# Performance work log

Measured on AMD Instinct MI355X. Metric: run time of the kernel, lower is better.

Reference implementation:

```python
import jax, jax.numpy as jnp
import numpy as np

TOP_K = 2
TEMP = 1.0

def setup_inputs() -> dict:
    key = jax.random.key(0)
    ks = jax.random.split(key, 7)
    B, T, D, E = 2, 2048, 768, 8
    F = 4 * D
    s = 0.02
    return {
        "x": jax.random.normal(ks[0], (B, T, D), dtype=jnp.float32),
        "gate_w": jax.random.normal(ks[1], (D, E), dtype=jnp.float32) * s,
        "gate_b": jnp.zeros((E,), dtype=jnp.float32),
        "w1": jax.random.normal(ks[2], (E, D, F), dtype=jnp.float32) * s,
        "b1": jnp.zeros((E, F), dtype=jnp.float32),
        "w2": jax.random.normal(ks[3], (E, F, D), dtype=jnp.float32) * s,
        "b2": jnp.zeros((E, D), dtype=jnp.float32),
    }

def reference(x, gate_w, gate_b, w1, b1, w2, b2):
    B, T, D = x.shape
    E = gate_w.shape[1]
    x_flat = x.reshape(-1, D)                       # [N, D]
    logits = x_flat @ gate_w + gate_b              # [N, E]
    gates = jax.nn.softmax(logits / TEMP, axis=-1)
    topk_gates, topk_idx = jax.lax.top_k(gates, TOP_K)   # [N, K]
    topk_gates = topk_gates / (jnp.sum(topk_gates, axis=-1, keepdims=True) + 1e-9)
    # Dense combine weights: w[n, e] = sum_k topk_gates[n, k] * (topk_idx[n, k] == e)
    combine = jnp.sum(
        topk_gates[:, :, None] * jax.nn.one_hot(topk_idx, E, dtype=x.dtype),
        axis=1,
    )                                               # [N, E]
    out = jnp.zeros_like(x_flat)
    for e in range(E):  # fixed small expert loop (structurally distinct params)
        h = jax.nn.gelu(x_flat @ w1[e] + b1[e], approximate=False)  # [N, 4D]
        y = h @ w2[e] + b2[e]                                       # [N, D]
        out = out + combine[:, e:e + 1] * y
    return out.reshape(B, T, D)
```

## Files before the change

### kernel.cpp

```cpp
#include <hip/hip_runtime.h>
#include <hip/hip_bf16.h>


#define N_TOK 4096
#define DIM   768
#define FDIM  3072
#define NEXP  8

typedef __attribute__((ext_vector_type(8))) _Float16 f16x8;
typedef __attribute__((ext_vector_type(4))) _Float16 f16x4;
typedef __attribute__((ext_vector_type(4))) float     f32x4;

__device__ __forceinline__ float gelu_exact(float v) {
    return 0.5f * v * (1.0f + erff(v * 0.7071067811865475f));
}

__device__ __forceinline__ void gload_lds16(const _Float16* g, _Float16* l) {
    __builtin_amdgcn_global_load_lds(
        (const __attribute__((address_space(1))) void*)g,
        (__attribute__((address_space(3))) void*)l,
        16, 0, 0);
}

__global__ __launch_bounds__(256) void cast_x_kernel(const float* __restrict__ x,
                                                     _Float16* __restrict__ xh) {
    int i = blockIdx.x * 256 + threadIdx.x;
    float4 v = ((const float4*)x)[i];
    f16x4 o;
    o[0] = (_Float16)v.x; o[1] = (_Float16)v.y;
    o[2] = (_Float16)v.z; o[3] = (_Float16)v.w;
    ((f16x4*)xh)[i] = o;
}

__global__ __launch_bounds__(256) void transpose_cast_kernel(const float* __restrict__ in,
                                                             _Float16* __restrict__ out,
                                                             int R, int C) {
    const int e  = blockIdx.z;
    const size_t eoff = (size_t)e * R * C;
    const int c0 = blockIdx.x * 64;
    const int r0 = blockIdx.y * 64;
    __shared__ _Float16 tile[64][66];
    const int t = threadIdx.x;
    #pragma unroll
    for (int it = 0; it < 4; it++) {
        int lin = it * 256 + t;
        int r  = lin >> 4;
        int c4 = lin & 15;
        float4 v = *(const float4*)&in[eoff + (size_t)(r0 + r) * C + c0 + c4 * 4];
        tile[r][c4 * 4 + 0] = (_Float16)v.x;
        tile[r][c4 * 4 + 1] = (_Float16)v.y;
        tile[r][c4 * 4 + 2] = (_Float16)v.z;
        tile[r][c4 * 4 + 3] = (_Float16)v.w;
    }
    __syncthreads();
    #pragma unroll
    for (int it = 0; it < 4; it++) {
        int lin = it * 256 + t;
        int c  = lin >> 4;
        int r4 = lin & 15;
        f16x4 o;
        #pragma unroll
        for (int j = 0; j < 4; j++) o[j] = tile[r4 * 4 + j][c];
        *(f16x4*)&out[eoff + (size_t)(c0 + c) * R + r0 + r4 * 4] = o;
    }
}

__global__ __launch_bounds__(256) void gate_kernel(const float* __restrict__ x,
                                                   const float* __restrict__ gw,
                                                   const float* __restrict__ gb,
                                                   int* __restrict__ tok_list,
                                                   float* __restrict__ wt_list,
                                                   int* __restrict__ count) {
    const int gtid = blockIdx.x * 256 + threadIdx.x;
    const int n    = gtid >> 6;
    const int lane = threadIdx.x & 63;
    if (n >= N_TOK) return;
    double part[NEXP];
    #pragma unroll
    for (int e = 0; e < NEXP; e++) part[e] = 0.0;
    for (int d = lane; d < DIM; d += 64) {
        float xv = x[n * DIM + d];
        const float* g = &gw[d * NEXP];
        #pragma unroll
        for (int e = 0; e < NEXP; e++) part[e] += (double)xv * (double)g[e];
    }
    #pragma unroll
    for (int e = 0; e < NEXP; e++) {
        double v = part[e];
        #pragma unroll
        for (int off = 32; off > 0; off >>= 1) v += __shfl_xor(v, off);
        part[e] = v + (double)gb[e];
    }
    if (lane == 0) {
        double mx = part[0];
        #pragma unroll
        for (int e = 1; e < NEXP; e++) mx = fmax(mx, part[e]);
        double ex[NEXP]; double s = 0.0;
        #pragma unroll
        for (int e = 0; e < NEXP; e++) { ex[e] = exp(part[e] - mx); s += ex[e]; }
        int i0 = 0;
        #pragma unroll
        for (int e = 1; e < NEXP; e++) if (ex[e] > ex[i0]) i0 = e;
        int i1 = (i0 == 0) ? 1 : 0;
        #pragma unroll
        for (int e = 0; e < NEXP; e++) if (e != i0 && ex[e] > ex[i1]) i1 = e;
        float g0 = (float)(ex[i0] / s), g1 = (float)(ex[i1] / s);
        float dn = g0 + g1 + 1e-9f;
        float w0 = g0 / dn, w1 = g1 / dn;
        int s0 = atomicAdd(&count[i0], 1);
        tok_list[i0 * N_TOK + s0] = n;  wt_list[i0 * N_TOK + s0] = w0;
        int s1 = atomicAdd(&count[i1], 1);
        tok_list[i1 * N_TOK + s1] = n;  wt_list[i1 * N_TOK + s1] = w1;
    }
}

__global__ void scan_kernel(const int* __restrict__ count, int* __restrict__ basep) {
    if (threadIdx.x == 0) {
        int s = 0;
        for (int e = 0; e < NEXP; e++) { basep[e] = s; s += count[e]; }
    }
}

__global__ __launch_bounds__(256) void mm1_kernel(const _Float16* __restrict__ xh,
                                                  const _Float16* __restrict__ w1t,
                                                  const float* __restrict__ bias1,
                                                  const int* __restrict__ tok_list,
                                                  const int* __restrict__ count,
                                                  const int* __restrict__ basep,
                                                  _Float16* __restrict__ h) {
    const int e    = blockIdx.y;
    const int cnt  = count[e];
    const int row0 = blockIdx.z * 128;
    if (row0 >= cnt) return;
    const int col0 = blockIdx.x * 128;
    const int t    = threadIdx.x;
    const int lane = t & 63;
    const int wv   = t >> 6;
    const int wy   = wv >> 1, wx = wv & 1;
    const int m_lane = lane & 15, quad = lane >> 4;

    __shared__ __align__(16) _Float16 As[128][32];
    __shared__ __align__(16) _Float16 Bs[128][32];

    const int srow = t >> 2;
    const int kin  = (t & 3) * 8;

    int i0 = row0 + srow;      if (i0 > cnt - 1) i0 = cnt - 1;
    int i1 = row0 + 64 + srow; if (i1 > cnt - 1) i1 = cnt - 1;
    const int tokA0 = tok_list[e * N_TOK + i0];
    const int tokA1 = tok_list[e * N_TOK + i1];
    const _Float16* pa0 = xh + (size_t)tokA0 * DIM + kin;
    const _Float16* pa1 = xh + (size_t)tokA1 * DIM + kin;
    const _Float16* pb0 = w1t + (size_t)e * FDIM * DIM + (size_t)(col0 + srow) * DIM + kin;
    const _Float16* pb1 = pb0 + (size_t)64 * DIM;

    f32x4 acc[4][4];
    #pragma unroll
    for (int i = 0; i < 4; i++)
        #pragma unroll
        for (int j = 0; j < 4; j++)
            acc[i][j] = (f32x4){0.f, 0.f, 0.f, 0.f};

    for (int kk = 0; kk < DIM; kk += 32) {
        __syncthreads();
        gload_lds16(pa0 + kk, &As[srow][kin]);
        gload_lds16(pa1 + kk, &As[64 + srow][kin]);
        gload_lds16(pb0 + kk, &Bs[srow][kin]);
        gload_lds16(pb1 + kk, &Bs[64 + srow][kin]);
        __syncthreads();
        f16x8 af[4], bf[4];
        #pragma unroll
        for (int i = 0; i < 4; i++)
            af[i] = *(const f16x8*)&As[wy * 64 + i * 16 + m_lane][quad * 8];
        #pragma unroll
        for (int j = 0; j < 4; j++)
            bf[j] = *(const f16x8*)&Bs[wx * 64 + j * 16 + m_lane][quad * 8];
        #pragma unroll
        for (int i = 0; i < 4; i++)
            #pragma unroll
            for (int j = 0; j < 4; j++)
                acc[i][j] = __builtin_amdgcn_mfma_f32_16x16x32_f16(af[i], bf[j], acc[i][j], 0, 0, 0);
    }

    const int hbase = basep[e];
    #pragma unroll
    for (int i = 0; i < 4; i++) {
        #pragma unroll
        for (int r = 0; r < 4; r++) {
            int rl = wy * 64 + i * 16 + quad * 4 + r;
            int gr = row0 + rl;
            if (gr < cnt) {
                _Float16* hrow = h + (size_t)(hbase + gr) * FDIM;
                #pragma unroll
                for (int j = 0; j < 4; j++) {
                    int c = col0 + wx * 64 + j * 16 + m_lane;
                    float v = acc[i][j][r] + bias1[e * FDIM + c];
                    hrow[c] = (_Float16)gelu_exact(v);
                }
            }
        }
    }
}

__global__ __launch_bounds__(256) void mm2_kernel(const _Float16* __restrict__ h,
                                                  const _Float16* __restrict__ w2t,
                                                  const float* __restrict__ bias2,
                                                  const int* __restrict__ tok_list,
                                                  const float* __restrict__ wt_list,
                                                  const int* __restrict__ count,
                                                  const int* __restrict__ basep,
                                                  float* __restrict__ out) {
    const int e    = blockIdx.y;
    const int cnt  = count[e];
    const int row0 = blockIdx.z * 128;
    if (row0 >= cnt) return;
    const int col0 = blockIdx.x * 128;
    const int t    = threadIdx.x;
    const int lane = t & 63;
    const int wv   = t >> 6;
    const int wy   = wv >> 1, wx = wv & 1;
    const int m_lane = lane & 15, quad = lane >> 4;

    __shared__ __align__(16) _Float16 As[128][32];
    __shared__ __align__(16) _Float16 Bs[128][32];

    const int srow = t >> 2;
    const int kin  = (t & 3) * 8;

    const int hbase = basep[e];
    int i0 = row0 + srow;      if (i0 > cnt - 1) i0 = cnt - 1;
    int i1 = row0 + 64 + srow; if (i1 > cnt - 1) i1 = cnt - 1;
    const _Float16* pa0 = h + (size_t)(hbase + i0) * FDIM + kin;
    const _Float16* pa1 = h + (size_t)(hbase + i1) * FDIM + kin;
    const _Float16* pb0 = w2t + (size_t)e * DIM * FDIM + (size_t)(col0 + srow) * FDIM + kin;
    const _Float16* pb1 = pb0 + (size_t)64 * FDIM;

    f32x4 acc[4][4];
    #pragma unroll
    for (int i = 0; i < 4; i++)
        #pragma unroll
        for (int j = 0; j < 4; j++)
            acc[i][j] = (f32x4){0.f, 0.f, 0.f, 0.f};

    for (int kk = 0; kk < FDIM; kk += 32) {
        __syncthreads();
        gload_lds16(pa0 + kk, &As[srow][kin]);
        gload_lds16(pa1 + kk, &As[64 + srow][kin]);
        gload_lds16(pb0 + kk, &Bs[srow][kin]);
        gload_lds16(pb1 + kk, &Bs[64 + srow][kin]);
        __syncthreads();
        f16x8 af[4], bf[4];
        #pragma unroll
        for (int i = 0; i < 4; i++)
            af[i] = *(const f16x8*)&As[wy * 64 + i * 16 + m_lane][quad * 8];
        #pragma unroll
        for (int j = 0; j < 4; j++)
            bf[j] = *(const f16x8*)&Bs[wx * 64 + j * 16 + m_lane][quad * 8];
        #pragma unroll
        for (int i = 0; i < 4; i++)
            #pragma unroll
            for (int j = 0; j < 4; j++)
                acc[i][j] = __builtin_amdgcn_mfma_f32_16x16x32_f16(af[i], bf[j], acc[i][j], 0, 0, 0);
    }

    #pragma unroll
    for (int i = 0; i < 4; i++) {
        #pragma unroll
        for (int r = 0; r < 4; r++) {
            int rl = wy * 64 + i * 16 + quad * 4 + r;
            int gr = row0 + rl;
            if (gr < cnt) {
                int tok   = tok_list[e * N_TOK + gr];
                float wgt = wt_list[e * N_TOK + gr];
                float* orow = out + (size_t)tok * DIM;
                #pragma unroll
                for (int j = 0; j < 4; j++) {
                    int c = col0 + wx * 64 + j * 16 + m_lane;
                    float v = acc[i][j][r] + bias2[e * DIM + c];
                    atomicAdd(&orow[c], wgt * v);
                }
            }
        }
    }
}

extern "C" void kernel_launch(void* const* d_in, const int* in_sizes, int n_in,
                              void* d_out, int out_size, void* d_ws, size_t ws_size,
                              hipStream_t stream) {
    const float* x  = (const float*)d_in[0];
    const float* gw = (const float*)d_in[1];
    const float* gb = (const float*)d_in[2];
    const float* w1 = (const float*)d_in[3];
    const float* b1 = (const float*)d_in[4];
    const float* w2 = (const float*)d_in[5];
    const float* b2 = (const float*)d_in[6];
    float* out = (float*)d_out;

    char* ws = (char*)d_ws;
    _Float16* xh   = (_Float16*)ws;
    _Float16* w1t  = xh  + (size_t)N_TOK * DIM;
    _Float16* w2t  = w1t + (size_t)NEXP * FDIM * DIM;
    _Float16* hbuf = w2t + (size_t)NEXP * DIM * FDIM;
    int*   tok_list = (int*)(hbuf + (size_t)2 * N_TOK * FDIM);
    float* wt_list  = (float*)(tok_list + NEXP * N_TOK);
    int*   count    = (int*)(wt_list + NEXP * N_TOK);
    int*   basep    = count + 8;

    hipMemsetAsync(count, 0, 64, stream);
    hipMemsetAsync(out, 0, (size_t)out_size * sizeof(float), stream);

    cast_x_kernel<<<dim3(N_TOK * DIM / 4 / 256), 256, 0, stream>>>(x, xh);
    transpose_cast_kernel<<<dim3(FDIM / 64, DIM / 64, NEXP), 256, 0, stream>>>(w1, w1t, DIM, FDIM);
    transpose_cast_kernel<<<dim3(DIM / 64, FDIM / 64, NEXP), 256, 0, stream>>>(w2, w2t, FDIM, DIM);
    gate_kernel<<<dim3(N_TOK / 4), 256, 0, stream>>>(x, gw, gb, tok_list, wt_list, count);
    scan_kernel<<<1, 64, 0, stream>>>(count, basep);
    mm1_kernel<<<dim3(FDIM / 128, NEXP, N_TOK / 128), 256, 0, stream>>>(
        xh, w1t, b1, tok_list, count, basep, hbuf);
    mm2_kernel<<<dim3(DIM / 128, NEXP, N_TOK / 128), 256, 0, stream>>>(
        hbuf, w2t, b2, tok_list, wt_list, count, basep, out);
}
```

Measured before the change: 493.9 us.

## Triple-buffer LDS loads in both expert GEMMs and split-K the second GEMM

Both grouped GEMM kernels now use a three-stage LDS ring. Async global-to-LDS loads for tile k+2 are issued while tile k is computed, with one barrier per iteration and vmcnt-based waits. This is meant to hide global load latency that the old two-barrier single-buffer loop exposed. The second GEMM is also split into two K halves on extra grid blocks to raise parallelism, since its grid was small (6 column tiles). That doubles the atomic adds into the output, and the bias is added only by the first half.

```diff
diff --git a/kernel.cpp b/kernel.cpp
--- a/kernel.cpp
+++ b/kernel.cpp
@@ -139,8 +139,8 @@
     const int wy   = wv >> 1, wx = wv & 1;
     const int m_lane = lane & 15, quad = lane >> 4;
 
-    __shared__ __align__(16) _Float16 As[128][32];
-    __shared__ __align__(16) _Float16 Bs[128][32];
+    __shared__ __align__(16) _Float16 As[3][128][32];
+    __shared__ __align__(16) _Float16 Bs[3][128][32];
 
     const int srow = t >> 2;
     const int kin  = (t & 3) * 8;
@@ -161,25 +161,45 @@
         for (int j = 0; j < 4; j++)
             acc[i][j] = (f32x4){0.f, 0.f, 0.f, 0.f};
 
-    for (int kk = 0; kk < DIM; kk += 32) {
-        __syncthreads();
-        gload_lds16(pa0 + kk, &As[srow][kin]);
-        gload_lds16(pa1 + kk, &As[64 + srow][kin]);
-        gload_lds16(pb0 + kk, &Bs[srow][kin]);
-        gload_lds16(pb1 + kk, &Bs[64 + srow][kin]);
-        __syncthreads();
+    const int NT = DIM / 32;
+
+    asm volatile("s_waitcnt vmcnt(0)" ::: "memory");
+    gload_lds16(pa0, &As[0][srow][kin]);
+    gload_lds16(pa1, &As[0][64 + srow][kin]);
+    gload_lds16(pb0, &Bs[0][srow][kin]);
+    gload_lds16(pb1, &Bs[0][64 + srow][kin]);
+    gload_lds16(pa0 + 32, &As[1][srow][kin]);
+    gload_lds16(pa1 + 32, &As[1][64 + srow][kin]);
+    gload_lds16(pb0 + 32, &Bs[1][srow][kin]);
+    gload_lds16(pb1 + 32, &Bs[1][64 + srow][kin]);
+
+    int cur = 0;
+    for (int ti = 0; ti < NT; ++ti) {
+        if (ti == NT - 1) asm volatile("s_waitcnt vmcnt(0) lgkmcnt(0)" ::: "memory");
+        else              asm volatile("s_waitcnt vmcnt(4) lgkmcnt(0)" ::: "memory");
+        __builtin_amdgcn_s_barrier();
+        asm volatile("" ::: "memory");
+        if (ti + 2 < NT) {
+            int nb = cur + 2; if (nb >= 3) nb -= 3;
+            int kk = (ti + 2) * 32;
+            gload_lds16(pa0 + kk, &As[nb][srow][kin]);
+            gload_lds16(pa1 + kk, &As[nb][64 + srow][kin]);
+            gload_lds16(pb0 + kk, &Bs[nb][srow][kin]);
+            gload_lds16(pb1 + kk, &Bs[nb][64 + srow][kin]);
+        }
         f16x8 af[4], bf[4];
         #pragma unroll
         for (int i = 0; i < 4; i++)
-            af[i] = *(const f16x8*)&As[wy * 64 + i * 16 + m_lane][quad * 8];
+            af[i] = *(const f16x8*)&As[cur][wy * 64 + i * 16 + m_lane][quad * 8];
         #pragma unroll
         for (int j = 0; j < 4; j++)
-            bf[j] = *(const f16x8*)&Bs[wx * 64 + j * 16 + m_lane][quad * 8];
+            bf[j] = *(const f16x8*)&Bs[cur][wx * 64 + j * 16 + m_lane][quad * 8];
         #pragma unroll
         for (int i = 0; i < 4; i++)
             #pragma unroll
             for (int j = 0; j < 4; j++)
                 acc[i][j] = __builtin_amdgcn_mfma_f32_16x16x32_f16(af[i], bf[j], acc[i][j], 0, 0, 0);
+        cur = cur + 1; if (cur >= 3) cur = 0;
     }
 
     const int hbase = basep[e];
@@ -210,7 +230,8 @@
                                                   const int* __restrict__ count,
                                                   const int* __restrict__ basep,
                                                   float* __restrict__ out) {
-    const int e    = blockIdx.y;
+    const int e    = blockIdx.y >> 1;
+    const int ks   = blockIdx.y & 1;
     const int cnt  = count[e];
     const int row0 = blockIdx.z * 128;
     if (row0 >= cnt) return;
@@ -221,8 +242,8 @@
     const int wy   = wv >> 1, wx = wv & 1;
     const int m_lane = lane & 15, quad = lane >> 4;
 
-    __shared__ __align__(16) _Float16 As[128][32];
-    __shared__ __align__(16) _Float16 Bs[128][32];
+    __shared__ __align__(16) _Float16 As[3][128][32];
+    __shared__ __align__(16) _Float16 Bs[3][128][32];
 
     const int srow = t >> 2;
     const int kin  = (t & 3) * 8;
@@ -230,9 +251,10 @@
     const int hbase = basep[e];
     int i0 = row0 + srow;      if (i0 > cnt - 1) i0 = cnt - 1;
     int i1 = row0 + 64 + srow; if (i1 > cnt - 1) i1 = cnt - 1;
-    const _Float16* pa0 = h + (size_t)(hbase + i0) * FDIM + kin;
-    const _Float16* pa1 = h + (size_t)(hbase + i1) * FDIM + kin;
-    const _Float16* pb0 = w2t + (size_t)e * DIM * FDIM + (size_t)(col0 + srow) * FDIM + kin;
+    const size_t koff = (size_t)ks * (FDIM / 2);
+    const _Float16* pa0 = h + (size_t)(hbase + i0) * FDIM + koff + kin;
+    const _Float16* pa1 = h + (size_t)(hbase + i1) * FDIM + koff + kin;
+    const _Float16* pb0 = w2t + (size_t)e * DIM * FDIM + (size_t)(col0 + srow) * FDIM + koff + kin;
     const _Float16* pb1 = pb0 + (size_t)64 * FDIM;
 
     f32x4 acc[4][4];
@@ -242,25 +264,45 @@
         for (int j = 0; j < 4; j++)
             acc[i][j] = (f32x4){0.f, 0.f, 0.f, 0.f};
 
-    for (int kk = 0; kk < FDIM; kk += 32) {
-        __syncthreads();
-        gload_lds16(pa0 + kk, &As[srow][kin]);
-        gload_lds16(pa1 + kk, &As[64 + srow][kin]);
-        gload_lds16(pb0 + kk, &Bs[srow][kin]);
-        gload_lds16(pb1 + kk, &Bs[64 + srow][kin]);
-        __syncthreads();
+    const int NT = (FDIM / 2) / 32;
+
+    asm volatile("s_waitcnt vmcnt(0)" ::: "memory");
+    gload_lds16(pa0, &As[0][srow][kin]);
+    gload_lds16(pa1, &As[0][64 + srow][kin]);
+    gload_lds16(pb0, &Bs[0][srow][kin]);
+    gload_lds16(pb1, &Bs[0][64 + srow][kin]);
+    gload_lds16(pa0 + 32, &As[1][srow][kin]);
+    gload_lds16(pa1 + 32, &As[1][64 + srow][kin]);
+    gload_lds16(pb0 + 32, &Bs[1][srow][kin]);
+    gload_lds16(pb1 + 32, &Bs[1][64 + srow][kin]);
+
+    int cur = 0;
+    for (int ti = 0; ti < NT; ++ti) {
+        if (ti == NT - 1) asm volatile("s_waitcnt vmcnt(0) lgkmcnt(0)" ::: "memory");
+        else              asm volatile("s_waitcnt vmcnt(4) lgkmcnt(0)" ::: "memory");
+        __builtin_amdgcn_s_barrier();
+        asm volatile("" ::: "memory");
+        if (ti + 2 < NT) {
+            int nb = cur + 2; if (nb >= 3) nb -= 3;
+            int kk = (ti + 2) * 32;
+            gload_lds16(pa0 + kk, &As[nb][srow][kin]);
+            gload_lds16(pa1 + kk, &As[nb][64 + srow][kin]);
+            gload_lds16(pb0 + kk, &Bs[nb][srow][kin]);
+            gload_lds16(pb1 + kk, &Bs[nb][64 + srow][kin]);
+        }
         f16x8 af[4], bf[4];
         #pragma unroll
         for (int i = 0; i < 4; i++)
-            af[i] = *(const f16x8*)&As[wy * 64 + i * 16 + m_lane][quad * 8];
+            af[i] = *(const f16x8*)&As[cur][wy * 64 + i * 16 + m_lane][quad * 8];
         #pragma unroll
         for (int j = 0; j < 4; j++)
-            bf[j] = *(const f16x8*)&Bs[wx * 64 + j * 16 + m_lane][quad * 8];
+            bf[j] = *(const f16x8*)&Bs[cur][wx * 64 + j * 16 + m_lane][quad * 8];
         #pragma unroll
         for (int i = 0; i < 4; i++)
             #pragma unroll
             for (int j = 0; j < 4; j++)
                 acc[i][j] = __builtin_amdgcn_mfma_f32_16x16x32_f16(af[i], bf[j], acc[i][j], 0, 0, 0);
+        cur = cur + 1; if (cur >= 3) cur = 0;
     }
 
     #pragma unroll
@@ -276,7 +318,7 @@
                 #pragma unroll
                 for (int j = 0; j < 4; j++) {
                     int c = col0 + wx * 64 + j * 16 + m_lane;
-                    float v = acc[i][j][r] + bias2[e * DIM + c];
+                    float v = acc[i][j][r] + ((ks == 0) ? bias2[e * DIM + c] : 0.f);
                     atomicAdd(&orow[c], wgt * v);
                 }
             }
@@ -316,6 +358,6 @@
     scan_kernel<<<1, 64, 0, stream>>>(count, basep);
     mm1_kernel<<<dim3(FDIM / 128, NEXP, N_TOK / 128), 256, 0, stream>>>(
         xh, w1t, b1, tok_list, count, basep, hbuf);
-    mm2_kernel<<<dim3(DIM / 128, NEXP, N_TOK / 128), 256, 0, stream>>>(
+    mm2_kernel<<<dim3(DIM / 128, NEXP * 2, N_TOK / 128), 256, 0, stream>>>(
         hbuf, w2t, b2, tok_list, wt_list, count, basep, out);
 }
```

Measured after the change: 556.7 us. +12.7%, slower.

## Double K-tile depth, shrink mm2 row tile, merge weight transpose launches

Applied to the files above, without the earlier changes.

Raises the per-iteration K depth of both expert GEMMs from 32 to 64, which halves the number of barrier pairs and makes each load phase larger. mm2 now uses 64-row tiles with each wave covering 32 columns, so more blocks run in the narrow N=768 output GEMM and the CUs are better filled. The two weight transpose-cast launches are merged into a single launch to remove one launch. In exchange, LDS per block doubles and mm2 reads each weight tile more often.

```diff
diff --git a/kernel.cpp b/kernel.cpp
--- a/kernel.cpp
+++ b/kernel.cpp
@@ -32,13 +32,19 @@
     ((f16x4*)xh)[i] = o;
 }
 
-__global__ __launch_bounds__(256) void transpose_cast_kernel(const float* __restrict__ in,
-                                                             _Float16* __restrict__ out,
-                                                             int R, int C) {
-    const int e  = blockIdx.z;
+__global__ __launch_bounds__(256) void transpose_cast2_kernel(const float* __restrict__ w1,
+                                                              const float* __restrict__ w2,
+                                                              _Float16* __restrict__ w1t,
+                                                              _Float16* __restrict__ w2t) {
+    const int z     = blockIdx.y;
+    const int which = z >> 3;
+    const int e     = z & 7;
+    const float* in; _Float16* out; int R, C, tx, ty;
+    if (which == 0) { in = w1; out = w1t; R = DIM;  C = FDIM; tx = blockIdx.x % (FDIM / 64); ty = blockIdx.x / (FDIM / 64); }
+    else            { in = w2; out = w2t; R = FDIM; C = DIM;  tx = blockIdx.x % (DIM  / 64); ty = blockIdx.x / (DIM  / 64); }
     const size_t eoff = (size_t)e * R * C;
-    const int c0 = blockIdx.x * 64;
-    const int r0 = blockIdx.y * 64;
+    const int c0 = tx * 64;
+    const int r0 = ty * 64;
     __shared__ _Float16 tile[64][66];
     const int t = threadIdx.x;
     #pragma unroll
@@ -139,20 +145,22 @@
     const int wy   = wv >> 1, wx = wv & 1;
     const int m_lane = lane & 15, quad = lane >> 4;
 
-    __shared__ __align__(16) _Float16 As[128][32];
-    __shared__ __align__(16) _Float16 Bs[128][32];
-
-    const int srow = t >> 2;
-    const int kin  = (t & 3) * 8;
-
-    int i0 = row0 + srow;      if (i0 > cnt - 1) i0 = cnt - 1;
-    int i1 = row0 + 64 + srow; if (i1 > cnt - 1) i1 = cnt - 1;
-    const int tokA0 = tok_list[e * N_TOK + i0];
-    const int tokA1 = tok_list[e * N_TOK + i1];
-    const _Float16* pa0 = xh + (size_t)tokA0 * DIM + kin;
-    const _Float16* pa1 = xh + (size_t)tokA1 * DIM + kin;
-    const _Float16* pb0 = w1t + (size_t)e * FDIM * DIM + (size_t)(col0 + srow) * DIM + kin;
-    const _Float16* pb1 = pb0 + (size_t)64 * DIM;
+    __shared__ __align__(16) _Float16 As[128][64];
+    __shared__ __align__(16) _Float16 Bs[128][64];
+
+    const int srow = t >> 3;
+    const int kin  = (t & 7) * 8;
+
+    const _Float16* pa[4];
+    #pragma unroll
+    for (int g = 0; g < 4; g++) {
+        int i = row0 + g * 32 + srow; if (i > cnt - 1) i = cnt - 1;
+        pa[g] = xh + (size_t)tok_list[e * N_TOK + i] * DIM + kin;
+    }
+    const _Float16* pb[4];
+    #pragma unroll
+    for (int g = 0; g < 4; g++)
+        pb[g] = w1t + (size_t)e * FDIM * DIM + (size_t)(col0 + g * 32 + srow) * DIM + kin;
 
     f32x4 acc[4][4];
     #pragma unroll
@@ -161,25 +169,28 @@
         for (int j = 0; j < 4; j++)
             acc[i][j] = (f32x4){0.f, 0.f, 0.f, 0.f};
 
-    for (int kk = 0; kk < DIM; kk += 32) {
+    for (int kk = 0; kk < DIM; kk += 64) {
         __syncthreads();
-        gload_lds16(pa0 + kk, &As[srow][kin]);
-        gload_lds16(pa1 + kk, &As[64 + srow][kin]);
-        gload_lds16(pb0 + kk, &Bs[srow][kin]);
-        gload_lds16(pb1 + kk, &Bs[64 + srow][kin]);
+        #pragma unroll
+        for (int g = 0; g < 4; g++) gload_lds16(pa[g] + kk, &As[g * 32 + srow][kin]);
+        #pragma unroll
+        for (int g = 0; g < 4; g++) gload_lds16(pb[g] + kk, &Bs[g * 32 + srow][kin]);
         __syncthreads();
-        f16x8 af[4], bf[4];
-        #pragma unroll
-        for (int i = 0; i < 4; i++)
-            af[i] = *(const f16x8*)&As[wy * 64 + i * 16 + m_lane][quad * 8];
-        #pragma unroll
-        for (int j = 0; j < 4; j++)
-            bf[j] = *(const f16x8*)&Bs[wx * 64 + j * 16 + m_lane][quad * 8];
-        #pragma unroll
-        for (int i = 0; i < 4; i++)
+        #pragma unroll
+        for (int ks = 0; ks < 2; ks++) {
+            f16x8 af[4], bf[4];
+            #pragma unroll
+            for (int i = 0; i < 4; i++)
+                af[i] = *(const f16x8*)&As[wy * 64 + i * 16 + m_lane][ks * 32 + quad * 8];
             #pragma unroll
             for (int j = 0; j < 4; j++)
-                acc[i][j] = __builtin_amdgcn_mfma_f32_16x16x32_f16(af[i], bf[j], acc[i][j], 0, 0, 0);
+                bf[j] = *(const f16x8*)&Bs[wx * 64 + j * 16 + m_lane][ks * 32 + quad * 8];
+            #pragma unroll
+            for (int i = 0; i < 4; i++)
+                #pragma unroll
+                for (int j = 0; j < 4; j++)
+                    acc[i][j] = __builtin_amdgcn_mfma_f32_16x16x32_f16(af[i], bf[j], acc[i][j], 0, 0, 0);
+        }
     }
 
     const int hbase = basep[e];
@@ -212,70 +223,76 @@
                                                   float* __restrict__ out) {
     const int e    = blockIdx.y;
     const int cnt  = count[e];
-    const int row0 = blockIdx.z * 128;
+    const int row0 = blockIdx.z * 64;
     if (row0 >= cnt) return;
     const int col0 = blockIdx.x * 128;
     const int t    = threadIdx.x;
     const int lane = t & 63;
     const int wv   = t >> 6;
-    const int wy   = wv >> 1, wx = wv & 1;
     const int m_lane = lane & 15, quad = lane >> 4;
 
-    __shared__ __align__(16) _Float16 As[128][32];
-    __shared__ __align__(16) _Float16 Bs[128][32];
-
-    const int srow = t >> 2;
-    const int kin  = (t & 3) * 8;
+    __shared__ __align__(16) _Float16 As[64][64];
+    __shared__ __align__(16) _Float16 Bs[128][64];
+
+    const int srow = t >> 3;
+    const int kin  = (t & 7) * 8;
 
     const int hbase = basep[e];
-    int i0 = row0 + srow;      if (i0 > cnt - 1) i0 = cnt - 1;
-    int i1 = row0 + 64 + srow; if (i1 > cnt - 1) i1 = cnt - 1;
-    const _Float16* pa0 = h + (size_t)(hbase + i0) * FDIM + kin;
-    const _Float16* pa1 = h + (size_t)(hbase + i1) * FDIM + kin;
-    const _Float16* pb0 = w2t + (size_t)e * DIM * FDIM + (size_t)(col0 + srow) * FDIM + kin;
-    const _Float16* pb1 = pb0 + (size_t)64 * FDIM;
-
-    f32x4 acc[4][4];
+    const _Float16* pa[2];
+    #pragma unroll
+    for (int g = 0; g < 2; g++) {
+        int i = row0 + g * 32 + srow; if (i > cnt - 1) i = cnt - 1;
+        pa[g] = h + (size_t)(hbase + i) * FDIM + kin;
+    }
+    const _Float16* pb[4];
+    #pragma unroll
+    for (int g = 0; g < 4; g++)
+        pb[g] = w2t + (size_t)e * DIM * FDIM + (size_t)(col0 + g * 32 + srow) * FDIM + kin;
+
+    f32x4 acc[4][2];
     #pragma unroll
     for (int i = 0; i < 4; i++)
         #pragma unroll
-        for (int j = 0; j < 4; j++)
+        for (int j = 0; j < 2; j++)
             acc[i][j] = (f32x4){0.f, 0.f, 0.f, 0.f};
 
-    for (int kk = 0; kk < FDIM; kk += 32) {
+    for (int kk = 0; kk < FDIM; kk += 64) {
         __syncthreads();
-        gload_lds16(pa0 + kk, &As[srow][kin]);
-        gload_lds16(pa1 + kk, &As[64 + srow][kin]);
-        gload_lds16(pb0 + kk, &Bs[srow][kin]);
-        gload_lds16(pb1 + kk, &Bs[64 + srow][kin]);
+        #pragma unroll
+        for (int g = 0; g < 2; g++) gload_lds16(pa[g] + kk, &As[g * 32 + srow][kin]);
+        #pragma unroll
+        for (int g = 0; g < 4; g++) gload_lds16(pb[g] + kk, &Bs[g * 32 + srow][kin]);
         __syncthreads();
-        f16x8 af[4], bf[4];
-        #pragma unroll
-        for (int i = 0; i < 4; i++)
-            af[i] = *(const f16x8*)&As[wy * 64 + i * 16 + m_lane][quad * 8];
-        #pragma unroll
-        for (int j = 0; j < 4; j++)
-            bf[j] = *(const f16x8*)&Bs[wx * 64 + j * 16 + m_lane][quad * 8];
-        #pragma unroll
-        for (int i = 0; i < 4; i++)
-            #pragma unroll
-            for (int j = 0; j < 4; j++)
-                acc[i][j] = __builtin_amdgcn_mfma_f32_16x16x32_f16(af[i], bf[j], acc[i][j], 0, 0, 0);
+        #pragma unroll
+        for (int ks = 0; ks < 2; ks++) {
+            f16x8 af[4], bf[2];
+            #pragma unroll
+            for (int i = 0; i < 4; i++)
+                af[i] = *(const f16x8*)&As[i * 16 + m_lane][ks * 32 + quad * 8];
+            #pragma unroll
+            for (int j = 0; j < 2; j++)
+                bf[j] = *(const f16x8*)&Bs[wv * 32 + j * 16 + m_lane][ks * 32 + quad * 8];
+            #pragma unroll
+            for (int i = 0; i < 4; i++)
+                #pragma unroll
+                for (int j = 0; j < 2; j++)
+                    acc[i][j] = __builtin_amdgcn_mfma_f32_16x16x32_f16(af[i], bf[j], acc[i][j], 0, 0, 0);
+        }
     }
 
     #pragma unroll
     for (int i = 0; i < 4; i++) {
         #pragma unroll
         for (int r = 0; r < 4; r++) {
-            int rl = wy * 64 + i * 16 + quad * 4 + r;
+            int rl = i * 16 + quad * 4 + r;
             int gr = row0 + rl;
             if (gr < cnt) {
                 int tok   = tok_list[e * N_TOK + gr];
                 float wgt = wt_list[e * N_TOK + gr];
                 float* orow = out + (size_t)tok * DIM;
                 #pragma unroll
-                for (int j = 0; j < 4; j++) {
-                    int c = col0 + wx * 64 + j * 16 + m_lane;
+                for (int j = 0; j < 2; j++) {
+                    int c = col0 + wv * 32 + j * 16 + m_lane;
                     float v = acc[i][j][r] + bias2[e * DIM + c];
                     atomicAdd(&orow[c], wgt * v);
                 }
@@ -310,12 +327,11 @@
     hipMemsetAsync(out, 0, (size_t)out_size * sizeof(float), stream);
 
     cast_x_kernel<<<dim3(N_TOK * DIM / 4 / 256), 256, 0, stream>>>(x, xh);
-    transpose_cast_kernel<<<dim3(FDIM / 64, DIM / 64, NEXP), 256, 0, stream>>>(w1, w1t, DIM, FDIM);
-    transpose_cast_kernel<<<dim3(DIM / 64, FDIM / 64, NEXP), 256, 0, stream>>>(w2, w2t, FDIM, DIM);
+    transpose_cast2_kernel<<<dim3(576, 16), 256, 0, stream>>>(w1, w2, w1t, w2t);
     gate_kernel<<<dim3(N_TOK / 4), 256, 0, stream>>>(x, gw, gb, tok_list, wt_list, count);
     scan_kernel<<<1, 64, 0, stream>>>(count, basep);
     mm1_kernel<<<dim3(FDIM / 128, NEXP, N_TOK / 128), 256, 0, stream>>>(
         xh, w1t, b1, tok_list, count, basep, hbuf);
-    mm2_kernel<<<dim3(DIM / 128, NEXP, N_TOK / 128), 256, 0, stream>>>(
+    mm2_kernel<<<dim3(DIM / 128, NEXP, N_TOK / 64), 256, 0, stream>>>(
         hbuf, w2t, b2, tok_list, wt_list, count, basep, out);
 }
```

Result: slower. 506.9 us (+2.6%).
